# Performance work log

Measured on AMD Instinct MI355X. Metric: run time of the kernel, lower is better.

Reference implementation:

```python
import jax, jax.numpy as jnp
import numpy as np

B, F = 512, 300  # F must satisfy F+4 == 16*19
EPS = 1e-5

def _leaky(v):
    return jnp.where(v >= 0, v, 0.01 * v)

def setup_inputs() -> dict:
    key = jax.random.key(0)
    ks = jax.random.split(key, 9)
    def conv_w(k, o, i):
        return jax.random.normal(k, (o, i), dtype=jnp.float32) * (1.0 / np.sqrt(i))
    x = jax.random.uniform(ks[0], (B, F), dtype=jnp.float32)
    return {
        "x": x,
        "w1": conv_w(ks[1], 256, 512), "b1": jnp.zeros((256,), jnp.float32),
        "w2": conv_w(ks[2], 128, 256), "b2": jnp.zeros((128,), jnp.float32),
        "w3": conv_w(ks[3], 64, 128),  "b3": jnp.zeros((64,), jnp.float32),
        "w4": conv_w(ks[4], 4, 64),    "b4": jnp.zeros((4,), jnp.float32),
    }

def reference(x, w1, b1, w2, b2, w3, b3, w4, b4):
    b = x.shape[0]
    xp = jnp.pad(x, ((0, 0), (2, 2)))                       # (b, 304)
    s1 = xp[:, None, :]                                      # unsqueeze(1)
    s2 = xp[:, :, None]                                      # unsqueeze(2)
    DI = s1 - s2                                             # (b,304,304)
    NDI = DI / (s1 + s2 + EPS)
    t = jnp.stack([DI, NDI], axis=-1)                        # (b,304,304,2)
    # tile into 16x16 grid of 19x19 patches, concat patches along channel
    # channel c = (row*16+col)*2 + d  (row-major loop order in original)
    t = t.reshape(b, 16, 19, 16, 19, 2).transpose(0, 2, 4, 1, 3, 5).reshape(b, 19, 19, 512)
    h = _leaky(jnp.einsum('bhwc,oc->bhwo', t, w1) + b1)      # (b,19,19,256)
    h = _leaky(jnp.einsum('bhwc,oc->bhwo', h, w2) + b2)      # (b,19,19,128)
    # masking branch (positional encoding in original is dead code / overwritten)
    m = jax.nn.relu(jnp.einsum('bhwc,oc->bhwo', h, w3) + b3)  # (b,19,19,64)
    m = jax.nn.relu(jnp.einsum('bhwc,oc->bhwo', m, w4) + b4)  # (b,19,19,4)
    m = m.transpose(3, 0, 1, 2).reshape(4, b, 19 * 19)
    m = jax.nn.softmax(m, axis=2).reshape(4, b, 19, 19, 1)
    # split 128 channels into 4 groups of 32
    g = h.reshape(b, 19, 19, 4, 32).transpose(3, 0, 1, 2, 4)  # (4,b,19,19,32)
    out = (g * m).sum(axis=(2, 3))                            # (4,b,32)
    return out.transpose(1, 0, 2).reshape(b, 128)
```

## Files before the change

### kernel.cpp

```cpp
#include <hip/hip_runtime.h>
#include <math.h>

typedef unsigned short ushort_t;
typedef __attribute__((ext_vector_type(8))) short short8;
typedef __attribute__((ext_vector_type(4))) float f32x4;

#define NTILES 12

#define WS_W_USHORTS 114688

__device__ inline ushort_t f2bf(float f) {
    unsigned u = __float_as_uint(f);
    return (ushort_t)((u + 0x7FFFu + ((u >> 16) & 1u)) >> 16);
}
__device__ inline unsigned pkbf(float f0, float f1) {
    unsigned a = __float_as_uint(f0) + 0x8000u;
    unsigned b = __float_as_uint(f1) + 0x8000u;
    return __builtin_amdgcn_perm(b, a, 0x07060302u);
}
__device__ inline float leaky(float v) { return fmaxf(v, 0.01f * v); }

__global__ void pack_weights(const float* __restrict__ w1, const float* __restrict__ w2,
                             const float* __restrict__ w3, ushort_t* __restrict__ ws) {
    const int idx = blockIdx.x * 256 + threadIdx.x;
    if (idx >= WS_W_USHORTS) return;
    float val = 0.f;
    if (idx < 73728) {
        const int j = idx & 7, lane = (idx >> 3) & 63, blk = idx >> 9;
        const int ks = blk % 9, os = blk / 9;
        const int m = lane & 15, q = lane >> 4;
        const int row = os * 16 + m;
        if (ks < 8) {
            const int k = ks * 32 + q * 8 + j;
            const int i1 = k >> 4, j1 = k & 15;
            val = w1[row * 512 + i1 * 32 + j1 * 2 + 1];
        } else {
            const int sub = q * 8 + j;
            if (sub < 16) {
                const int j1 = sub;
                float s = 0.f;
                #pragma unroll
                for (int i1 = 0; i1 < 16; ++i1) s += w1[row * 512 + i1 * 32 + j1 * 2];
                val = s;
            } else {
                const int i1 = sub - 16;
                float s = 0.f;
                #pragma unroll
                for (int j1 = 0; j1 < 16; ++j1) s += w1[row * 512 + i1 * 32 + j1 * 2];
                val = -s;
            }
        }
    } else if (idx < 106496) {
        const int l = idx - 73728;
        const int j = l & 7, lane = (l >> 3) & 63, blk = l >> 9;
        const int ks = blk & 7, os = blk >> 3;
        const int m = lane & 15, q = lane >> 4;
        val = w2[(os * 16 + m) * 256 + ks * 32 + q * 8 + j];
    } else {
        const int l = idx - 106496;
        const int j = l & 7, lane = (l >> 3) & 63, blk = l >> 9;
        const int ks = blk & 3, os = blk >> 2;
        const int m = lane & 15, q = lane >> 4;
        val = w3[(os * 16 + m) * 128 + ks * 32 + q * 8 + j];
    }
    ws[idx] = f2bf(val);
}

template <int NS>
__global__ __launch_bounds__(512, 4) void fused_mfma(
    const float* __restrict__ x, const ushort_t* __restrict__ ws,
    const float* __restrict__ b1, const float* __restrict__ b2,
    const float* __restrict__ b3, const float* __restrict__ b4,
    const float* __restrict__ w4,
    float* __restrict__ partA, float* __restrict__ partS)
{
    __shared__ __align__(16) ushort_t sm[19048];
    ushort_t* const ts   = sm;
    ushort_t* const h2s  = sm;
    ushort_t* const h1s  = sm + 10240;
    float*   const wbuf  = (float*)(sm + 10240);
    float*   const xp    = (float*)(sm + 18432);

    constexpr int SH  = (NS == 4) ? 2 : ((NS == 2) ? 1 : 0);
    constexpr int TPS = (NTILES + NS - 1) / NS;
    const int tid = threadIdx.x;
    const int s   = blockIdx.x & (NS - 1);
    const int bb  = blockIdx.x >> SH;
    const int t0  = s * TPS;
    const int t1  = (t0 + TPS < NTILES) ? (t0 + TPS) : NTILES;

    const int wv   = tid >> 6;
    const int lane = tid & 63;
    const int n0   = lane & 15;
    const int qi   = lane >> 4;
    const int sx   = n0 & 7;
    const int row0 = qi * 4;
    const int o3s  = wv & 3;
    const int ps3  = wv >> 2;
    const int qh   = wv >> 1;

    for (int jj = tid; jj < 308; jj += 512) {
        float v = 0.f;
        const int src = jj - 2;
        if (src >= 0 && src < 300) v = x[bb * 300 + src];
        xp[jj] = v;
    }

    const short8* wf1 = (const short8*)(ws);
    const short8* wf2 = (const short8*)(ws + 73728);
    const short8* wf3 = (const short8*)(ws + 106496);

    f32x4 bv1[2], bv2, bv3;
    #pragma unroll
    for (int jo = 0; jo < 2; ++jo) bv1[jo] = *(const f32x4*)&b1[(wv * 2 + jo) * 16 + row0];
    bv2 = *(const f32x4*)&b2[wv * 16 + row0];
    bv3 = *(const f32x4*)&b3[o3s * 16 + row0];
    const float b4s = b4[qh];

    f32x4 Afr[2] = {{0.f, 0.f, 0.f, 0.f}, {0.f, 0.f, 0.f, 0.f}};
    float Ss = 0.f;

    __syncthreads();

    for (int tile = t0; tile < t1; ++tile) {
        const int pos0 = tile * 32;

        {
            const int p  = tid & 31;
            const int i1 = tid >> 5;
            int posg = pos0 + p; if (posg > 360) posg = 360;
            const int hh = posg / 19;
            const int ww = posg - 19 * hh;
            const int base = p * 320;
            const int psw  = p & 7;
            const float v = xp[i1 * 19 + hh];
            float u[16];
            #pragma unroll
            for (int j1 = 0; j1 < 16; ++j1) u[j1] = xp[j1 * 19 + ww];
            #pragma unroll
            for (int j1 = 0; j1 < 16; j1 += 2) {
                const float nd0 = (u[j1] - v)     * __builtin_amdgcn_rcpf(u[j1] + v + 1e-5f);
                const float nd1 = (u[j1 + 1] - v) * __builtin_amdgcn_rcpf(u[j1 + 1] + v + 1e-5f);
                const int oct = i1 * 2 + (j1 >> 3);
                *(unsigned*)&ts[base + ((oct ^ psw) << 3) + (j1 & 7)] = pkbf(nd0, nd1);
            }
            if (i1 == 0) {
                #pragma unroll
                for (int j1 = 0; j1 < 16; j1 += 2) {
                    const int oct = 32 + (j1 >> 3);
                    *(unsigned*)&ts[base + ((oct ^ psw) << 3) + (j1 & 7)] = pkbf(u[j1], u[j1 + 1]);
                }
            } else if (i1 == 1) {
                #pragma unroll
                for (int i2 = 0; i2 < 16; i2 += 2) {
                    const float v0 = xp[i2 * 19 + hh];
                    const float v1 = xp[(i2 + 1) * 19 + hh];
                    const int oct = 34 + (i2 >> 3);
                    *(unsigned*)&ts[base + ((oct ^ psw) << 3) + (i2 & 7)] = pkbf(v0, v1);
                }
            }
        }
        __syncthreads();

        {
            f32x4 acc[2][2];
            #pragma unroll
            for (int jo = 0; jo < 2; ++jo) { acc[jo][0] = bv1[jo]; acc[jo][1] = bv1[jo]; }
            const int tb0 = n0 * 320;
            const int tb1 = tb0 + 16 * 320;
            const int wbase = wv * 1152 + lane;
            #pragma unroll 3
            for (int ks = 0; ks < 9; ++ks) {
                const int oct = ks * 4 + qi;
                const short8 bb0 = *(const short8*)&ts[tb0 + ((oct ^ sx) << 3)];
                const short8 bb1 = *(const short8*)&ts[tb1 + ((oct ^ sx) << 3)];
                #pragma unroll
                for (int jo = 0; jo < 2; ++jo) {
                    const short8 a = wf1[wbase + (jo * 9 + ks) * 64];
                    acc[jo][0] = __builtin_amdgcn_mfma_f32_16x16x32_bf16(a, bb0, acc[jo][0], 0, 0, 0);
                    acc[jo][1] = __builtin_amdgcn_mfma_f32_16x16x32_bf16(a, bb1, acc[jo][1], 0, 0, 0);
                }
            }
            #pragma unroll
            for (int jo = 0; jo < 2; ++jo) {
                const int out0 = (wv * 2 + jo) * 16 + row0;
                #pragma unroll
                for (int ps = 0; ps < 2; ++ps) {
                    const f32x4 a4 = acc[jo][ps];
                    uint2 pk;
                    pk.x = pkbf(leaky(a4.x), leaky(a4.y));
                    pk.y = pkbf(leaky(a4.z), leaky(a4.w));
                    *(uint2*)&h1s[(ps * 16 + n0) * 256 + (((out0 >> 3) ^ sx) << 3) + (out0 & 7)] = pk;
                }
            }
        }
        __syncthreads();

        f32x4 h2f[2];
        {
            f32x4 acc[2] = {bv2, bv2};
            const int hb0 = n0 * 256;
            const int hb1 = hb0 + 16 * 256;
            #pragma unroll 4
            for (int ks = 0; ks < 8; ++ks) {
                const int oct = ks * 4 + qi;
                const short8 bb0 = *(const short8*)&h1s[hb0 + ((oct ^ sx) << 3)];
                const short8 bb1 = *(const short8*)&h1s[hb1 + ((oct ^ sx) << 3)];
                const short8 a = wf2[(wv * 8 + ks) * 64 + lane];
                acc[0] = __builtin_amdgcn_mfma_f32_16x16x32_bf16(a, bb0, acc[0], 0, 0, 0);
                acc[1] = __builtin_amdgcn_mfma_f32_16x16x32_bf16(a, bb1, acc[1], 0, 0, 0);
            }
            const int out0 = wv * 16 + row0;
            #pragma unroll
            for (int ps = 0; ps < 2; ++ps) {
                f32x4 a4 = acc[ps];
                a4.x = leaky(a4.x); a4.y = leaky(a4.y);
                a4.z = leaky(a4.z); a4.w = leaky(a4.w);
                h2f[ps] = a4;
                uint2 pk;
                pk.x = pkbf(a4.x, a4.y);
                pk.y = pkbf(a4.z, a4.w);
                *(uint2*)&h2s[(ps * 16 + n0) * 128 + (((out0 >> 3) ^ sx) << 3) + (out0 & 7)] = pk;
            }
        }
        __syncthreads();

        {
            f32x4 acc = bv3;
            const int cb = (ps3 * 16 + n0) * 128;
            #pragma unroll
            for (int ks = 0; ks < 4; ++ks) {
                const int oct = ks * 4 + qi;
                const short8 bbv = *(const short8*)&h2s[cb + ((oct ^ sx) << 3)];
                const short8 a = wf3[(o3s * 4 + ks) * 64 + lane];
                acc = __builtin_amdgcn_mfma_f32_16x16x32_bf16(a, bbv, acc, 0, 0, 0);
            }
            f32x4 m3 = acc;
            m3.x = fmaxf(m3.x, 0.f); m3.y = fmaxf(m3.y, 0.f);
            m3.z = fmaxf(m3.z, 0.f); m3.w = fmaxf(m3.w, 0.f);
            float pl[4];
            #pragma unroll
            for (int q = 0; q < 4; ++q) {
                const f32x4 w4r = *(const f32x4*)&w4[q * 64 + o3s * 16 + row0];
                pl[q] = w4r.x * m3.x + w4r.y * m3.y + w4r.z * m3.z + w4r.w * m3.w;
            }
            #pragma unroll
            for (int q = 0; q < 4; ++q) {
                pl[q] += __shfl_xor(pl[q], 16, 64);
                pl[q] += __shfl_xor(pl[q], 32, 64);
            }
            if (qi == 0) {
                #pragma unroll
                for (int q = 0; q < 4; ++q)
                    wbuf[(o3s * 4 + q) * 32 + ps3 * 16 + n0] = pl[q];
            }
        }
        __syncthreads();

        {
            #pragma unroll
            for (int ps = 0; ps < 2; ++ps) {
                const int pos = ps * 16 + n0;
                float lg = wbuf[(0 * 4 + qh) * 32 + pos] + wbuf[(1 * 4 + qh) * 32 + pos]
                         + wbuf[(2 * 4 + qh) * 32 + pos] + wbuf[(3 * 4 + qh) * 32 + pos] + b4s;
                lg = fmaxf(lg, 0.f);
                const float e = ((pos0 + pos) > 360) ? 0.f : __expf(lg);
                Afr[ps].x += e * h2f[ps].x;
                Afr[ps].y += e * h2f[ps].y;
                Afr[ps].z += e * h2f[ps].z;
                Afr[ps].w += e * h2f[ps].w;
                Ss += e;
            }
        }
    }

    f32x4 At;
    At.x = Afr[0].x + Afr[1].x; At.y = Afr[0].y + Afr[1].y;
    At.z = Afr[0].z + Afr[1].z; At.w = Afr[0].w + Afr[1].w;
    #pragma unroll
    for (int bit = 1; bit < 16; bit <<= 1) {
        At.x += __shfl_xor(At.x, bit, 64);
        At.y += __shfl_xor(At.y, bit, 64);
        At.z += __shfl_xor(At.z, bit, 64);
        At.w += __shfl_xor(At.w, bit, 64);
        Ss += __shfl_xor(Ss, bit, 64);
    }
    if (n0 == 0) {
        const int pbA = (s * 512 + bb) * 128 + wv * 16 + row0;
        partA[pbA]     = At.x;
        partA[pbA + 1] = At.y;
        partA[pbA + 2] = At.z;
        partA[pbA + 3] = At.w;
        if (qi == 0 && (wv & 1) == 0) partS[(s * 512 + bb) * 4 + qh] = Ss;
    }
}

template <int NS>
__global__ void merge_out(const float* __restrict__ partA, const float* __restrict__ partS,
                          float* __restrict__ out) {
    const int idx = blockIdx.x * 256 + threadIdx.x;
    if (idx >= 512 * 128) return;
    const int bb = idx >> 7, ch = idx & 127;
    const int q = ch >> 5;
    float Sf = 0.f, Af = 0.f;
    #pragma unroll
    for (int s = 0; s < NS; ++s) {
        Af += partA[(s * 512 + bb) * 128 + ch];
        Sf += partS[(s * 512 + bb) * 4 + q];
    }
    out[idx] = Af / Sf;
}

__global__ __launch_bounds__(256, 2) void fallback_fused(
    const float* __restrict__ x,
    const float* __restrict__ w1, const float* __restrict__ b1,
    const float* __restrict__ w2, const float* __restrict__ b2,
    const float* __restrict__ w3, const float* __restrict__ b3,
    const float* __restrict__ w4, const float* __restrict__ b4,
    float* __restrict__ out)
{
    __shared__ float smf[14644];
    float* const xp  = smf;
    float* const ts  = smf + 308;
    float* const h1s = smf + 8500;
    float* const h2s = smf + 12596;
    float* const m3s = ts;
    float* const lgs = ts + 1024;

    const int tid = threadIdx.x;
    const int b   = blockIdx.x;
    for (int j = tid; j < 308; j += 256) {
        float v = 0.f;
        const int src = j - 2;
        if (src >= 0 && src < 300) v = x[b * 300 + src];
        xp[j] = v;
    }
    __syncthreads();
    const int q = tid >> 5, dd = tid & 31;
    float M = -1e30f, S = 0.f, A = 0.f;
    for (int tile = 0; tile < 23; ++tile) {
        const int pos0 = tile * 16;
        {
            const int p = tid & 15, kk0 = tid >> 4;
            const int pos = pos0 + p;
            const bool valid = (pos < 361);
            const int hh = valid ? (pos / 19) : 0;
            const int ww = valid ? (pos - hh * 19) : 0;
            #pragma unroll
            for (int i = 0; i < 16; ++i) {
                const int kk = kk0 + (i << 4);
                const int i1 = kk >> 4, j1 = kk & 15;
                float di = 0.f, ndi = 0.f;
                if (valid) {
                    const float u = xp[j1 * 19 + ww];
                    const float v = xp[i1 * 19 + hh];
                    di = u - v; ndi = di / (u + v + 1e-5f);
                }
                ts[(kk << 5) + p] = di;
                ts[(kk << 5) + 16 + p] = ndi;
            }
        }
        __syncthreads();
        {
            const int o = tid;
            float acc[16];
            const float bias = b1[o];
            #pragma unroll
            for (int p = 0; p < 16; ++p) acc[p] = bias;
            for (int k = 0; k < 512; ++k) {
                const float wv = w1[o * 512 + k];
                #pragma unroll
                for (int p = 0; p < 16; ++p) acc[p] += wv * ts[(k << 4) + p];
            }
            #pragma unroll
            for (int p = 0; p < 16; ++p) h1s[(o << 4) + p] = (acc[p] >= 0.f) ? acc[p] : 0.01f * acc[p];
        }
        __syncthreads();
        {
            const int o2 = tid & 127, pb = (tid >> 7) << 3;
            float acc[8];
            const float bias = b2[o2];
            #pragma unroll
            for (int j = 0; j < 8; ++j) acc[j] = bias;
            for (int k = 0; k < 256; ++k) {
                const float wv = w2[o2 * 256 + k];
                #pragma unroll
                for (int j = 0; j < 8; ++j) acc[j] += wv * h1s[(k << 4) + pb + j];
            }
            #pragma unroll
            for (int j = 0; j < 8; ++j) h2s[(o2 << 4) + pb + j] = (acc[j] >= 0.f) ? acc[j] : 0.01f * acc[j];
        }
        __syncthreads();
        {
            const int o3 = tid & 63, pb = (tid >> 6) << 2;
            float acc[4];
            const float bias = b3[o3];
            #pragma unroll
            for (int j = 0; j < 4; ++j) acc[j] = bias;
            for (int k = 0; k < 128; ++k) {
                const float wv = w3[o3 * 128 + k];
                #pragma unroll
                for (int j = 0; j < 4; ++j) acc[j] += wv * h2s[(k << 4) + pb + j];
            }
            #pragma unroll
            for (int j = 0; j < 4; ++j) m3s[(o3 << 4) + pb + j] = fmaxf(acc[j], 0.f);
        }
        __syncthreads();
        if (tid < 64) {
            const int o4 = tid >> 4, p = tid & 15;
            float a = b4[o4];
            for (int k = 0; k < 64; ++k) a += w4[o4 * 64 + k] * m3s[(k << 4) + p];
            a = fmaxf(a, 0.f);
            if (pos0 + p >= 361) a = -1e30f;
            lgs[(o4 << 4) + p] = a;
        }
        __syncthreads();
        if (tid < 128) {
            float l[16];
            #pragma unroll
            for (int p = 0; p < 16; ++p) l[p] = lgs[(q << 4) + p];
            float tmax = l[0];
            #pragma unroll
            for (int p = 1; p < 16; ++p) tmax = fmaxf(tmax, l[p]);
            const float newM = fmaxf(M, tmax);
            const float alpha = __expf(M - newM);
            float ssum = 0.f, asum = 0.f;
            #pragma unroll
            for (int p = 0; p < 16; ++p) {
                const float e = __expf(l[p] - newM);
                ssum += e;
                asum += e * h2s[(((q << 5) + dd) << 4) + p];
            }
            S = S * alpha + ssum; A = A * alpha + asum; M = newM;
        }
        __syncthreads();
    }
    if (tid < 128) out[(b << 7) + tid] = A / S;
}

extern "C" void kernel_launch(void* const* d_in, const int* in_sizes, int n_in,
                              void* d_out, int out_size, void* d_ws, size_t ws_size,
                              hipStream_t stream) {
    const float* x  = (const float*)d_in[0];
    const float* w1 = (const float*)d_in[1];
    const float* b1 = (const float*)d_in[2];
    const float* w2 = (const float*)d_in[3];
    const float* b2 = (const float*)d_in[4];
    const float* w3 = (const float*)d_in[5];
    const float* b3 = (const float*)d_in[6];
    const float* w4 = (const float*)d_in[7];
    const float* b4 = (const float*)d_in[8];
    float* out = (float*)d_out;

    const size_t wbytes = (size_t)WS_W_USHORTS * sizeof(ushort_t);
    ushort_t* ws = (ushort_t*)d_ws;
    const int packBlocks = (WS_W_USHORTS + 255) / 256;

    const size_t need4 = wbytes + (size_t)4 * 512 * 132 * sizeof(float);
    const size_t need2 = wbytes + (size_t)2 * 512 * 132 * sizeof(float);
    const size_t need1 = wbytes + (size_t)1 * 512 * 132 * sizeof(float);

    if (ws_size >= need4) {
        float* pA = (float*)((char*)d_ws + wbytes);
        float* pS = pA + (size_t)4 * 512 * 128;
        pack_weights<<<packBlocks, 256, 0, stream>>>(w1, w2, w3, ws);
        fused_mfma<4><<<2048, 512, 0, stream>>>(x, ws, b1, b2, b3, b4, w4, pA, pS);
        merge_out<4><<<256, 256, 0, stream>>>(pA, pS, out);
    } else if (ws_size >= need2) {
        float* pA = (float*)((char*)d_ws + wbytes);
        float* pS = pA + (size_t)2 * 512 * 128;
        pack_weights<<<packBlocks, 256, 0, stream>>>(w1, w2, w3, ws);
        fused_mfma<2><<<1024, 512, 0, stream>>>(x, ws, b1, b2, b3, b4, w4, pA, pS);
        merge_out<2><<<256, 256, 0, stream>>>(pA, pS, out);
    } else if (ws_size >= need1) {
        float* pA = (float*)((char*)d_ws + wbytes);
        float* pS = pA + (size_t)1 * 512 * 128;
        pack_weights<<<packBlocks, 256, 0, stream>>>(w1, w2, w3, ws);
        fused_mfma<1><<<512, 512, 0, stream>>>(x, ws, b1, b2, b3, b4, w4, pA, pS);
        merge_out<1><<<256, 256, 0, stream>>>(pA, pS, out);
    } else {
        fallback_fused<<<512, 256, 0, stream>>>(x, w1, b1, w2, b2, w3, b3, w4, b4, out);
    }
}
```

Before: 150.4 us.

## Change LDS swizzle pattern, vectorize tile stores, and drop four-way position split

Replaces the row&7 XOR swizzle with a (r + r>>3)&7 swizzle so the two 16-row halves of each tile use different XOR keys, which is meant to reduce LDS bank conflicts on the MFMA operand reads and result writes. The per-thread tile build now packs eight bf16 values into one 128-bit LDS store instead of four 32-bit stores. The launcher also drops the NS=4 path, so it uses two position slices per batch row (1024 blocks) with fewer partial sums to merge, at the cost of less parallelism per batch.

```diff
diff --git a/kernel.cpp b/kernel.cpp
--- a/kernel.cpp
+++ b/kernel.cpp
@@ -19,6 +19,7 @@
     return __builtin_amdgcn_perm(b, a, 0x07060302u);
 }
 __device__ inline float leaky(float v) { return fmaxf(v, 0.01f * v); }
+__device__ inline int sxf(int r) { return (r + (r >> 3)) & 7; }
 
 __global__ void pack_weights(const float* __restrict__ w1, const float* __restrict__ w2,
                              const float* __restrict__ w3, ushort_t* __restrict__ ws) {
@@ -93,10 +94,12 @@
     const int lane = tid & 63;
     const int n0   = lane & 15;
     const int qi   = lane >> 4;
-    const int sx   = n0 & 7;
+    const int sx0  = sxf(n0);
+    const int sx1  = sxf(n0 + 16);
     const int row0 = qi * 4;
     const int o3s  = wv & 3;
     const int ps3  = wv >> 2;
+    const int sx3  = ps3 ? sx1 : sx0;
     const int qh   = wv >> 1;
 
     for (int jj = tid; jj < 308; jj += 512) {
@@ -132,31 +135,49 @@
             const int hh = posg / 19;
             const int ww = posg - 19 * hh;
             const int base = p * 320;
-            const int psw  = p & 7;
+            const int psw  = sxf(p);
             const float v = xp[i1 * 19 + hh];
             float u[16];
             #pragma unroll
             for (int j1 = 0; j1 < 16; ++j1) u[j1] = xp[j1 * 19 + ww];
             #pragma unroll
-            for (int j1 = 0; j1 < 16; j1 += 2) {
-                const float nd0 = (u[j1] - v)     * __builtin_amdgcn_rcpf(u[j1] + v + 1e-5f);
-                const float nd1 = (u[j1 + 1] - v) * __builtin_amdgcn_rcpf(u[j1 + 1] + v + 1e-5f);
-                const int oct = i1 * 2 + (j1 >> 3);
-                *(unsigned*)&ts[base + ((oct ^ psw) << 3) + (j1 & 7)] = pkbf(nd0, nd1);
+            for (int jb = 0; jb < 16; jb += 8) {
+                uint4 wq;
+                unsigned* wp = (unsigned*)&wq;
+                #pragma unroll
+                for (int jj = 0; jj < 8; jj += 2) {
+                    const int j1 = jb + jj;
+                    const float nd0 = (u[j1] - v)     * __builtin_amdgcn_rcpf(u[j1] + v + 1e-5f);
+                    const float nd1 = (u[j1 + 1] - v) * __builtin_amdgcn_rcpf(u[j1 + 1] + v + 1e-5f);
+                    wp[jj >> 1] = pkbf(nd0, nd1);
+                }
+                const int oct = i1 * 2 + (jb >> 3);
+                *(uint4*)&ts[base + ((oct ^ psw) << 3)] = wq;
             }
             if (i1 == 0) {
                 #pragma unroll
-                for (int j1 = 0; j1 < 16; j1 += 2) {
-                    const int oct = 32 + (j1 >> 3);
-                    *(unsigned*)&ts[base + ((oct ^ psw) << 3) + (j1 & 7)] = pkbf(u[j1], u[j1 + 1]);
+                for (int jb = 0; jb < 16; jb += 8) {
+                    uint4 wq;
+                    unsigned* wp = (unsigned*)&wq;
+                    #pragma unroll
+                    for (int jj = 0; jj < 8; jj += 2)
+                        wp[jj >> 1] = pkbf(u[jb + jj], u[jb + jj + 1]);
+                    const int oct = 32 + (jb >> 3);
+                    *(uint4*)&ts[base + ((oct ^ psw) << 3)] = wq;
                 }
             } else if (i1 == 1) {
                 #pragma unroll
-                for (int i2 = 0; i2 < 16; i2 += 2) {
-                    const float v0 = xp[i2 * 19 + hh];
-                    const float v1 = xp[(i2 + 1) * 19 + hh];
-                    const int oct = 34 + (i2 >> 3);
-                    *(unsigned*)&ts[base + ((oct ^ psw) << 3) + (i2 & 7)] = pkbf(v0, v1);
+                for (int ib = 0; ib < 16; ib += 8) {
+                    uint4 wq;
+                    unsigned* wp = (unsigned*)&wq;
+                    #pragma unroll
+                    for (int ii = 0; ii < 8; ii += 2) {
+                        const float v0 = xp[(ib + ii) * 19 + hh];
+                        const float v1 = xp[(ib + ii + 1) * 19 + hh];
+                        wp[ii >> 1] = pkbf(v0, v1);
+                    }
+                    const int oct = 34 + (ib >> 3);
+                    *(uint4*)&ts[base + ((oct ^ psw) << 3)] = wq;
                 }
             }
         }
@@ -172,8 +193,8 @@
             #pragma unroll 3
             for (int ks = 0; ks < 9; ++ks) {
                 const int oct = ks * 4 + qi;
-                const short8 bb0 = *(const short8*)&ts[tb0 + ((oct ^ sx) << 3)];
-                const short8 bb1 = *(const short8*)&ts[tb1 + ((oct ^ sx) << 3)];
+                const short8 bb0 = *(const short8*)&ts[tb0 + ((oct ^ sx0) << 3)];
+                const short8 bb1 = *(const short8*)&ts[tb1 + ((oct ^ sx1) << 3)];
                 #pragma unroll
                 for (int jo = 0; jo < 2; ++jo) {
                     const short8 a = wf1[wbase + (jo * 9 + ks) * 64];
@@ -190,7 +211,8 @@
                     uint2 pk;
                     pk.x = pkbf(leaky(a4.x), leaky(a4.y));
                     pk.y = pkbf(leaky(a4.z), leaky(a4.w));
-                    *(uint2*)&h1s[(ps * 16 + n0) * 256 + (((out0 >> 3) ^ sx) << 3) + (out0 & 7)] = pk;
+                    const int sxw = ps ? sx1 : sx0;
+                    *(uint2*)&h1s[(ps * 16 + n0) * 256 + (((out0 >> 3) ^ sxw) << 3) + (out0 & 7)] = pk;
                 }
             }
         }
@@ -204,8 +226,8 @@
             #pragma unroll 4
             for (int ks = 0; ks < 8; ++ks) {
                 const int oct = ks * 4 + qi;
-                const short8 bb0 = *(const short8*)&h1s[hb0 + ((oct ^ sx) << 3)];
-                const short8 bb1 = *(const short8*)&h1s[hb1 + ((oct ^ sx) << 3)];
+                const short8 bb0 = *(const short8*)&h1s[hb0 + ((oct ^ sx0) << 3)];
+                const short8 bb1 = *(const short8*)&h1s[hb1 + ((oct ^ sx1) << 3)];
                 const short8 a = wf2[(wv * 8 + ks) * 64 + lane];
                 acc[0] = __builtin_amdgcn_mfma_f32_16x16x32_bf16(a, bb0, acc[0], 0, 0, 0);
                 acc[1] = __builtin_amdgcn_mfma_f32_16x16x32_bf16(a, bb1, acc[1], 0, 0, 0);
@@ -220,7 +242,8 @@
                 uint2 pk;
                 pk.x = pkbf(a4.x, a4.y);
                 pk.y = pkbf(a4.z, a4.w);
-                *(uint2*)&h2s[(ps * 16 + n0) * 128 + (((out0 >> 3) ^ sx) << 3) + (out0 & 7)] = pk;
+                const int sxw = ps ? sx1 : sx0;
+                *(uint2*)&h2s[(ps * 16 + n0) * 128 + (((out0 >> 3) ^ sxw) << 3) + (out0 & 7)] = pk;
             }
         }
         __syncthreads();
@@ -231,7 +254,7 @@
             #pragma unroll
             for (int ks = 0; ks < 4; ++ks) {
                 const int oct = ks * 4 + qi;
-                const short8 bbv = *(const short8*)&h2s[cb + ((oct ^ sx) << 3)];
+                const short8 bbv = *(const short8*)&h2s[cb + ((oct ^ sx3) << 3)];
                 const short8 a = wf3[(o3s * 4 + ks) * 64 + lane];
                 acc = __builtin_amdgcn_mfma_f32_16x16x32_bf16(a, bbv, acc, 0, 0, 0);
             }
@@ -456,17 +479,10 @@
     ushort_t* ws = (ushort_t*)d_ws;
     const int packBlocks = (WS_W_USHORTS + 255) / 256;
 
-    const size_t need4 = wbytes + (size_t)4 * 512 * 132 * sizeof(float);
     const size_t need2 = wbytes + (size_t)2 * 512 * 132 * sizeof(float);
     const size_t need1 = wbytes + (size_t)1 * 512 * 132 * sizeof(float);
 
-    if (ws_size >= need4) {
-        float* pA = (float*)((char*)d_ws + wbytes);
-        float* pS = pA + (size_t)4 * 512 * 128;
-        pack_weights<<<packBlocks, 256, 0, stream>>>(w1, w2, w3, ws);
-        fused_mfma<4><<<2048, 512, 0, stream>>>(x, ws, b1, b2, b3, b4, w4, pA, pS);
-        merge_out<4><<<256, 256, 0, stream>>>(pA, pS, out);
-    } else if (ws_size >= need2) {
+    if (ws_size >= need2) {
         float* pA = (float*)((char*)d_ws + wbytes);
         float* pS = pA + (size_t)2 * 512 * 128;
         pack_weights<<<packBlocks, 256, 0, stream>>>(w1, w2, w3, ws);
```

Result: slower. 159.6 us (+6.1%).
